# Performance work log

Hardware: AMD Instinct MI355X
Metric: run time of the kernel (lower is better)

The kernel has to match this reference:

```python
import jax, jax.numpy as jnp
from jax import lax
import numpy as np

H = W = 2048
C = 3
KSIZE = 2
SIGMA = 2.0
ITERATIONS = 2
RADII = (256.0, 768.0)
# with max_displacement=0 all circle centers coincide, so 'close to any circle'
# reduces to distance^2 < max(radius^2)
SRADII_MAX = max(r ** 2 for r in RADII)
SCLEAN_MAX = max(max(r - KSIZE, 0.0) ** 2 for r in RADII)


def _gaussian_blur(x, sigma):
    """skimage.filters.gaussian equivalent: separable gaussian, truncate=4.0,
    mode='nearest' (edge padding), channel_axis=-1 (no blur across channels)."""
    radius = int(4.0 * sigma + 0.5)
    t = np.arange(-radius, radius + 1, dtype=np.float32)
    k = np.exp(-0.5 * (t / sigma) ** 2)
    k = (k / k.sum()).astype(np.float32)
    for axis in (0, 1):
        pad = [(0, 0)] * x.ndim
        pad[axis] = (radius, radius)
        xp = jnp.pad(x, pad, mode='edge')
        n = x.shape[axis]
        acc = jnp.zeros_like(x)
        for j in range(k.shape[0]):
            acc = acc + k[j] * lax.slice_in_dim(xp, j, j + n, axis=axis)
        x = acc
    return x


def _glass_forward(img, offsets):
    r = KSIZE
    Hv = H - 2 * r + 1  # loop range(r, H-r+1) -> H-2r+1 rows
    Wv = W - 2 * r + 1
    HWtot = H * W
    # original quirk: cx = shape[0]//2 compared against column index w,
    # cy = shape[1]//2 against row index h; identical for a square image.
    cx = H // 2
    cy = W // 2
    ys = jnp.arange(r, H - r + 1)
    xs = jnp.arange(r, W - r + 1)
    HH, WW = jnp.meshgrid(ys, xs, indexing='ij')  # (Hv, Wv)
    d2 = (cx - WW) ** 2 + (cy - HH) ** 2
    swap_mask = (d2 >= SRADII_MAX).reshape(-1)  # swap only OUTSIDE all circles
    local = ((HH - r) * Wv + (WW - r)).reshape(-1)  # raster order within loop
    lin = (HH * W + WW).reshape(-1)

    # Every read in the original swap loop comes from array_orig (never
    # updated), so the final value of each pixel equals array_orig[source]
    # where source is determined by the LAST write targeting that pixel.
    # Each loop step emits two ordered writes:
    #   array[h, w]   = orig[h_, w_]   (order = 2*raster)
    #   array[h_, w_] = orig[h, w]    (order = 2*raster + 1)
    # We replay this exactly with a scatter-max over write order.
    writes = []
    for i in range(ITERATIONS):
        dh = offsets[i, :, :, 0]
        dw = offsets[i, :, :, 1]
        lin_ = ((HH + dh) * W + (WW + dw)).reshape(-1)
        base = i * 2 * Hv * Wv
        o1 = base + 2 * local
        o2 = o1 + 1
        writes.append((lin, lin_, o1))
        writes.append((lin_, lin, o2))

    win = jnp.full((HWtot,), -1, jnp.int32)
    for tgt, src_idx, order in writes:
        win = win.at[tgt].max(jnp.where(swap_mask, order, -1))
    src = jnp.full((HWtot,), -1, jnp.int32)
    for tgt, src_idx, order in writes:
        hit = swap_mask & (order == win[tgt])
        src = src.at[tgt].max(jnp.where(hit, src_idx, -1))

    orig_flat = img.reshape(HWtot, C)
    gathered = orig_flat[jnp.maximum(src, 0)]
    swapped = jnp.where((src >= 0)[:, None], gathered, orig_flat).reshape(H, W, C)

    blurred = jnp.clip(_gaussian_blur(swapped / 255.0, SIGMA), 0.0, 1.0) * 255.0

    # restore original pixels close to the shrunken (clean) circles
    clean = d2 < SCLEAN_MAX  # (Hv, Wv)
    clean_full = jnp.zeros((H, W), bool).at[r:H - r + 1, r:W - r + 1].set(clean)
    return jnp.where(clean_full[:, :, None], img, blurred)


def setup_inputs() -> dict:
    key = jax.random.key(0)
    k1, k2 = jax.random.split(key)
    img = jax.random.uniform(k1, (H, W, C), jnp.float32) * 255.0
    offsets = jax.random.randint(
        k2, (ITERATIONS, H - 2 * KSIZE + 1, W - 2 * KSIZE + 1, 2),
        -KSIZE, KSIZE, dtype=jnp.int32)
    return {"img": img, "offsets": offsets}


def reference(img, offsets):
    return _glass_forward(img, offsets)
```

## Files before the change

### kernel.cpp

```cpp
#include <hip/hip_runtime.h>
#include <hip/hip_fp16.h>

#define Hh 2048
#define Ww 2048
#define HW (2048 * 2048)
constexpr int REG = 2045;
constexpr int RBASE = 2 * 2045 * 2045;
constexpr int SWAP_D2 = 589824;
constexpr int CLEAN_D2 = 586756;

__device__ __constant__ float GK[17] = {
    6.691628e-05f, 4.363490e-04f, 2.215963e-03f, 8.764304e-03f,
    2.699596e-02f, 6.475994e-02f, 1.209875e-01f, 1.760358e-01f,
    1.9947466e-01f, 1.760358e-01f, 1.209875e-01f, 6.475994e-02f,
    2.699596e-02f, 8.764304e-03f, 2.215963e-03f, 4.363490e-04f,
    6.691628e-05f};

constexpr int TX = 32, TY = 8;
constexpr int HX = TX + 3, HY = TY + 3;

__global__ __launch_bounds__(256) void swap_gather(
    const float* __restrict__ img, const int* __restrict__ off,
    __half* __restrict__ A) {
  int x0 = blockIdx.x * TX, y0 = blockIdx.y * TY;
  int tx = threadIdx.x & 31, ty = threadIdx.x >> 5;
  int px = x0 + tx, py = y0 + ty;
  int plin = py * Ww + px;
  int src = plin;

  int mxx = max(abs(1024 - (x0 - 1)), abs(1024 - (x0 + TX + 1)));
  int mxy = max(abs(1024 - (y0 - 1)), abs(1024 - (y0 + TY + 1)));
  if (mxx * mxx + mxy * mxy >= SWAP_D2) {
    __shared__ int4 sh[HY * HX];
    for (int e = threadIdx.x; e < HY * HX; e += 256) {
      int ly = e / HX, lx = e - ly * HX;
      int qy = y0 - 1 + ly, qx = x0 - 1 + lx;
      int4 v = make_int4(100, 100, 100, 100);
      int dcx = 1024 - qx, dcy = 1024 - qy;
      if (qy >= 2 && qy <= 2046 && qx >= 2 && qx <= 2046 &&
          dcx * dcx + dcy * dcy >= SWAP_D2) {
        int base = ((qy - 2) * REG + (qx - 2)) * 2;
        const int2 a0 = *(const int2*)&off[base];
        const int2 a1 = *(const int2*)&off[RBASE + base];
        v = make_int4(a0.x, a0.y, a1.x, a1.y);
      }
      sh[e] = v;
    }
    __syncthreads();

    int best = -1;
    int base0 = 2 * ((py - 2) * REG + (px - 2)) + 1;
    {
      int dcx = 1024 - px, dcy = 1024 - py;
      if (px >= 2 && px <= 2046 && py >= 2 && py <= 2046 &&
          dcx * dcx + dcy * dcy >= SWAP_D2) {
        best = RBASE + base0 - 1;
        int4 v = sh[(ty + 1) * HX + (tx + 1)];
        src = plin + v.z * Ww + v.w;
      }
    }
#pragma unroll
    for (int dyi = 0; dyi < 4; ++dyi) {
      int ddy = 1 - dyi;
#pragma unroll
      for (int dxi = 0; dxi < 4; ++dxi) {
        int ddx = 1 - dxi;
        int4 v = sh[(ty + dyi) * HX + (tx + dxi)];
        int ordc = base0 - 2 * (ddy * REG + ddx);
        int qlin = plin - ddy * Ww - ddx;
        bool h0 = (v.x == ddy) & (v.y == ddx);
        bool h1 = (v.z == ddy) & (v.w == ddx);
        if (h0 & (ordc > best)) { best = ordc; src = qlin; }
        int ord1 = ordc + RBASE;
        if (h1 & (ord1 > best)) { best = ord1; src = qlin; }
      }
    }
  }

  float r = img[src * 3 + 0];
  float g = img[src * 3 + 1];
  float b = img[src * 3 + 2];
  A[plin] = __float2half(r);
  A[HW + plin] = __float2half(g);
  A[2 * HW + plin] = __float2half(b);
}

constexpr int YPT = 16;
__global__ void vblur(const __half* __restrict__ A, __half* __restrict__ B) {
  int x0 = (blockIdx.x * 256 + threadIdx.x) * 2;
  int y0 = blockIdx.y * YPT;
  const __half* Ap = A + (size_t)blockIdx.z * HW;
  __half* Bp = B + (size_t)blockIdx.z * HW;
  float2 acc[YPT];
#pragma unroll
  for (int k = 0; k < YPT; ++k) acc[k] = make_float2(0.f, 0.f);
#pragma unroll
  for (int j = 0; j < YPT + 16; ++j) {
    int ys = y0 - 8 + j;
    ys = ys < 0 ? 0 : (ys > Hh - 1 ? Hh - 1 : ys);
    __half2 h = *(const __half2*)&Ap[ys * Ww + x0];
    float2 v = __half22float2(h);
#pragma unroll
    for (int k = 0; k < YPT; ++k) {
      int t = j - k;
      if (t >= 0 && t <= 16) {
        acc[k].x += GK[t] * v.x;
        acc[k].y += GK[t] * v.y;
      }
    }
  }
#pragma unroll
  for (int k = 0; k < YPT; ++k) {
    *(__half2*)&Bp[(y0 + k) * Ww + x0] = __float22half2_rn(acc[k]);
  }
}

__global__ void hblur_compose(const __half* __restrict__ B,
                              const float* __restrict__ img,
                              float* __restrict__ out) {
  __shared__ float tile[256 + 16];
  int tid = threadIdx.x;
  int xs = blockIdx.x * 256;
  int y = blockIdx.y;
  int x = xs + tid;
  float br[3];
  for (int c = 0; c < 3; ++c) {
    const __half* Bp = B + (size_t)c * HW + (size_t)y * Ww;
    __syncthreads();
    int xg = xs - 8 + tid;
    xg = xg < 0 ? 0 : (xg > Ww - 1 ? Ww - 1 : xg);
    tile[tid] = __half2float(Bp[xg]);
    if (tid < 16) {
      int xg2 = xs - 8 + 256 + tid;
      xg2 = xg2 > Ww - 1 ? Ww - 1 : xg2;
      tile[256 + tid] = __half2float(Bp[xg2]);
    }
    __syncthreads();
    float s = 0.f;
#pragma unroll
    for (int j = 0; j < 17; ++j) s += GK[j] * tile[tid + j];
    br[c] = s;
  }
  int dx = 1024 - x, dy = 1024 - y;
  int d2 = dx * dx + dy * dy;
  bool clean = (x >= 2 && x <= 2046 && y >= 2 && y <= 2046 && d2 < CLEAN_D2);
  int p3 = (y * Ww + x) * 3;
  if (clean) {
    out[p3 + 0] = img[p3 + 0];
    out[p3 + 1] = img[p3 + 1];
    out[p3 + 2] = img[p3 + 2];
  } else {
#pragma unroll
    for (int c = 0; c < 3; ++c) {
      float v = br[c];
      v = v < 0.f ? 0.f : (v > 255.f ? 255.f : v);
      out[p3 + c] = v;
    }
  }
}

extern "C" void kernel_launch(void* const* d_in, const int* in_sizes, int n_in,
                              void* d_out, int out_size, void* d_ws,
                              size_t ws_size, hipStream_t stream) {
  const float* img = (const float*)d_in[0];
  const int* off = (const int*)d_in[1];
  float* out = (float*)d_out;

  __half* A = (__half*)d_ws;
  __half* Bp = A + (size_t)3 * HW;

  swap_gather<<<dim3(Ww / TX, Hh / TY), 256, 0, stream>>>(img, off, A);
  vblur<<<dim3(4, Hh / YPT, 3), 256, 0, stream>>>(A, Bp);
  hblur_compose<<<dim3(Ww / 256, Hh), 256, 0, stream>>>(Bp, img, out);
}
```

Baseline: 187.5 us.

## Pack swap offsets into bytes, order-based candidate scan, widen blur vectors

```diff
diff --git a/kernel.cpp b/kernel.cpp
--- a/kernel.cpp
+++ b/kernel.cpp
@@ -26,57 +26,67 @@
   int tx = threadIdx.x & 31, ty = threadIdx.x >> 5;
   int px = x0 + tx, py = y0 + ty;
   int plin = py * Ww + px;
-  int src = plin;
+  int srcoff = 0;
 
   int mxx = max(abs(1024 - (x0 - 1)), abs(1024 - (x0 + TX + 1)));
   int mxy = max(abs(1024 - (y0 - 1)), abs(1024 - (y0 + TY + 1)));
   if (mxx * mxx + mxy * mxy >= SWAP_D2) {
-    __shared__ int4 sh[HY * HX];
+    __shared__ unsigned sh[HY * HX];
     for (int e = threadIdx.x; e < HY * HX; e += 256) {
       int ly = e / HX, lx = e - ly * HX;
       int qy = y0 - 1 + ly, qx = x0 - 1 + lx;
-      int4 v = make_int4(100, 100, 100, 100);
+      unsigned v = 0xFFFFFFFFu;
       int dcx = 1024 - qx, dcy = 1024 - qy;
       if (qy >= 2 && qy <= 2046 && qx >= 2 && qx <= 2046 &&
           dcx * dcx + dcy * dcy >= SWAP_D2) {
         int base = ((qy - 2) * REG + (qx - 2)) * 2;
         const int2 a0 = *(const int2*)&off[base];
         const int2 a1 = *(const int2*)&off[RBASE + base];
-        v = make_int4(a0.x, a0.y, a1.x, a1.y);
+        v = (unsigned)(a0.y + 2) | ((unsigned)(a0.x + 2) << 8) |
+            ((unsigned)(a1.y + 2) << 16) | ((unsigned)(a1.x + 2) << 24);
       }
       sh[e] = v;
     }
     __syncthreads();
 
-    int best = -1;
-    int base0 = 2 * ((py - 2) * REG + (px - 2)) + 1;
+    unsigned w[4][4];
+#pragma unroll
+    for (int dyi = 0; dyi < 4; ++dyi)
+#pragma unroll
+      for (int dxi = 0; dxi < 4; ++dxi)
+        w[dyi][dxi] = sh[(ty + dyi) * HX + (tx + dxi)];
+
+#define CANDC(dyi, dxi) ((unsigned)((1 - (dxi)) + 2) | ((unsigned)((1 - (dyi)) + 2) << 8))
+#define OFFC(dyi, dxi) (-(1 - (dyi)) * Ww - (1 - (dxi)))
+#define CAND0(dyi, dxi) \
+  if ((w[dyi][dxi] & 0xFFFFu) == CANDC(dyi, dxi)) srcoff = OFFC(dyi, dxi);
+#define CAND1(dyi, dxi) \
+  if ((w[dyi][dxi] >> 16) == CANDC(dyi, dxi)) srcoff = OFFC(dyi, dxi);
+
+    CAND0(0, 0) CAND0(0, 1) CAND0(0, 2) CAND0(0, 3)
+    CAND0(1, 0) CAND0(1, 1) CAND0(1, 2) CAND0(1, 3)
+    CAND0(2, 0) CAND0(2, 1) CAND0(2, 2) CAND0(2, 3)
+    CAND0(3, 0) CAND0(3, 1) CAND0(3, 2) CAND0(3, 3)
+    CAND1(0, 0) CAND1(0, 1) CAND1(0, 2) CAND1(0, 3)
+    CAND1(1, 0)
     {
-      int dcx = 1024 - px, dcy = 1024 - py;
-      if (px >= 2 && px <= 2046 && py >= 2 && py <= 2046 &&
-          dcx * dcx + dcy * dcy >= SWAP_D2) {
-        best = RBASE + base0 - 1;
-        int4 v = sh[(ty + 1) * HX + (tx + 1)];
-        src = plin + v.z * Ww + v.w;
-      }
-    }
-#pragma unroll
-    for (int dyi = 0; dyi < 4; ++dyi) {
-      int ddy = 1 - dyi;
-#pragma unroll
-      for (int dxi = 0; dxi < 4; ++dxi) {
-        int ddx = 1 - dxi;
-        int4 v = sh[(ty + dyi) * HX + (tx + dxi)];
-        int ordc = base0 - 2 * (ddy * REG + ddx);
-        int qlin = plin - ddy * Ww - ddx;
-        bool h0 = (v.x == ddy) & (v.y == ddx);
-        bool h1 = (v.z == ddy) & (v.w == ddx);
-        if (h0 & (ordc > best)) { best = ordc; src = qlin; }
-        int ord1 = ordc + RBASE;
-        if (h1 & (ord1 > best)) { best = ord1; src = qlin; }
-      }
-    }
-  }
-
+      unsigned wc = w[1][1];
+      if ((wc >> 24) != 0xFFu) {
+        int dh1 = (int)((wc >> 24) & 0xFFu) - 2;
+        int dw1 = (int)((wc >> 16) & 0xFFu) - 2;
+        srcoff = dh1 * Ww + dw1;
+      }
+    }
+    CAND1(1, 1) CAND1(1, 2) CAND1(1, 3)
+    CAND1(2, 0) CAND1(2, 1) CAND1(2, 2) CAND1(2, 3)
+    CAND1(3, 0) CAND1(3, 1) CAND1(3, 2) CAND1(3, 3)
+#undef CANDC
+#undef OFFC
+#undef CAND0
+#undef CAND1
+  }
+
+  int src = plin + srcoff;
   float r = img[src * 3 + 0];
   float g = img[src * 3 + 1];
   float b = img[src * 3 + 2];
@@ -86,75 +96,114 @@
 }
 
 constexpr int YPT = 16;
-__global__ void vblur(const __half* __restrict__ A, __half* __restrict__ B) {
-  int x0 = (blockIdx.x * 256 + threadIdx.x) * 2;
-  int y0 = blockIdx.y * YPT;
-  const __half* Ap = A + (size_t)blockIdx.z * HW;
-  __half* Bp = B + (size_t)blockIdx.z * HW;
-  float2 acc[YPT];
-#pragma unroll
-  for (int k = 0; k < YPT; ++k) acc[k] = make_float2(0.f, 0.f);
+__global__ __launch_bounds__(256) void vblur(const __half* __restrict__ A,
+                                             __half* __restrict__ B) {
+  int b = blockIdx.x;
+  int xcd = b & 7, r = b >> 3;
+  int ystrip = (xcd << 4) | (r & 15);
+  int rem = r >> 4;
+  int xb = rem & 1, c = rem >> 1;
+  int x0 = (xb * 256 + threadIdx.x) * 4;
+  int y0 = ystrip * YPT;
+  const __half* Ap = A + (size_t)c * HW;
+  __half* Bp = B + (size_t)c * HW;
+
+  float acc[YPT][4];
+#pragma unroll
+  for (int k = 0; k < YPT; ++k)
+#pragma unroll
+    for (int q = 0; q < 4; ++q) acc[k][q] = 0.f;
+
 #pragma unroll
   for (int j = 0; j < YPT + 16; ++j) {
     int ys = y0 - 8 + j;
     ys = ys < 0 ? 0 : (ys > Hh - 1 ? Hh - 1 : ys);
-    __half2 h = *(const __half2*)&Ap[ys * Ww + x0];
-    float2 v = __half22float2(h);
+    uint2 raw = *(const uint2*)&Ap[(size_t)ys * Ww + x0];
+    __half2 h01 = *(__half2*)&raw.x;
+    __half2 h23 = *(__half2*)&raw.y;
+    float2 v01 = __half22float2(h01);
+    float2 v23 = __half22float2(h23);
 #pragma unroll
     for (int k = 0; k < YPT; ++k) {
       int t = j - k;
       if (t >= 0 && t <= 16) {
-        acc[k].x += GK[t] * v.x;
-        acc[k].y += GK[t] * v.y;
+        float gk = GK[t];
+        acc[k][0] += gk * v01.x;
+        acc[k][1] += gk * v01.y;
+        acc[k][2] += gk * v23.x;
+        acc[k][3] += gk * v23.y;
       }
     }
   }
 #pragma unroll
   for (int k = 0; k < YPT; ++k) {
-    *(__half2*)&Bp[(y0 + k) * Ww + x0] = __float22half2_rn(acc[k]);
-  }
-}
-
-__global__ void hblur_compose(const __half* __restrict__ B,
-                              const float* __restrict__ img,
-                              float* __restrict__ out) {
-  __shared__ float tile[256 + 16];
+    uint2 o;
+    __half2 h01 = __float22half2_rn(make_float2(acc[k][0], acc[k][1]));
+    __half2 h23 = __float22half2_rn(make_float2(acc[k][2], acc[k][3]));
+    o.x = *(unsigned*)&h01;
+    o.y = *(unsigned*)&h23;
+    *(uint2*)&Bp[(size_t)(y0 + k) * Ww + x0] = o;
+  }
+}
+
+__global__ __launch_bounds__(256) void hblur_compose(
+    const __half* __restrict__ B, const float* __restrict__ img,
+    float* __restrict__ out) {
+  __shared__ float tile[528 + 1];
   int tid = threadIdx.x;
-  int xs = blockIdx.x * 256;
+  int xs = blockIdx.x * 512;
   int y = blockIdx.y;
-  int x = xs + tid;
-  float br[3];
+  float br[3][2];
+
   for (int c = 0; c < 3; ++c) {
     const __half* Bp = B + (size_t)c * HW + (size_t)y * Ww;
     __syncthreads();
-    int xg = xs - 8 + tid;
-    xg = xg < 0 ? 0 : (xg > Ww - 1 ? Ww - 1 : xg);
-    tile[tid] = __half2float(Bp[xg]);
-    if (tid < 16) {
-      int xg2 = xs - 8 + 256 + tid;
-      xg2 = xg2 > Ww - 1 ? Ww - 1 : xg2;
-      tile[256 + tid] = __half2float(Bp[xg2]);
+    for (int e = tid; e < 264; e += 256) {
+      int xg = xs - 8 + 2 * e;
+      float2 v;
+      if (xg >= 0 && xg + 1 <= Ww - 1) {
+        __half2 h = *(const __half2*)&Bp[xg];
+        v = __half22float2(h);
+      } else {
+        int xlo = xg < 0 ? 0 : (xg > Ww - 1 ? Ww - 1 : xg);
+        int xhi = xg + 1 < 0 ? 0 : (xg + 1 > Ww - 1 ? Ww - 1 : xg + 1);
+        v = make_float2(__half2float(Bp[xlo]), __half2float(Bp[xhi]));
+      }
+      *(float2*)&tile[2 * e] = v;
     }
     __syncthreads();
-    float s = 0.f;
-#pragma unroll
-    for (int j = 0; j < 17; ++j) s += GK[j] * tile[tid + j];
-    br[c] = s;
-  }
-  int dx = 1024 - x, dy = 1024 - y;
-  int d2 = dx * dx + dy * dy;
-  bool clean = (x >= 2 && x <= 2046 && y >= 2 && y <= 2046 && d2 < CLEAN_D2);
-  int p3 = (y * Ww + x) * 3;
-  if (clean) {
-    out[p3 + 0] = img[p3 + 0];
-    out[p3 + 1] = img[p3 + 1];
-    out[p3 + 2] = img[p3 + 2];
-  } else {
-#pragma unroll
-    for (int c = 0; c < 3; ++c) {
-      float v = br[c];
-      v = v < 0.f ? 0.f : (v > 255.f ? 255.f : v);
-      out[p3 + c] = v;
+    float f[19];
+#pragma unroll
+    for (int j = 0; j < 19; ++j) f[j] = tile[2 * tid + j];
+    float s0 = 0.f, s1 = 0.f;
+#pragma unroll
+    for (int j = 0; j < 17; ++j) {
+      s0 += GK[j] * f[j];
+      s1 += GK[j] * f[j + 1];
+    }
+    br[c][0] = s0;
+    br[c][1] = s1;
+  }
+
+  int x = xs + 2 * tid;
+#pragma unroll
+  for (int u = 0; u < 2; ++u) {
+    int xu = x + u;
+    int dx = 1024 - xu, dy = 1024 - y;
+    bool clean = (xu >= 2 && xu <= 2046 && y >= 2 && y <= 2046 &&
+                  dx * dx + dy * dy < CLEAN_D2);
+    int p3 = (y * Ww + xu) * 3;
+    if (clean) {
+      out[p3 + 0] = img[p3 + 0];
+      out[p3 + 1] = img[p3 + 1];
+      out[p3 + 2] = img[p3 + 2];
+    } else {
+#pragma unroll
+      for (int c = 0; c < 3; ++c) {
+        float v = br[c][u];
+        v = v < 0.f ? 0.f : (v > 255.f ? 255.f : v);
+        out[p3 + c] = v;
+      }
     }
   }
 }
@@ -170,6 +219,6 @@
   __half* Bp = A + (size_t)3 * HW;
 
   swap_gather<<<dim3(Ww / TX, Hh / TY), 256, 0, stream>>>(img, off, A);
-  vblur<<<dim3(4, Hh / YPT, 3), 256, 0, stream>>>(A, Bp);
-  hblur_compose<<<dim3(Ww / 256, Hh), 256, 0, stream>>>(Bp, img, out);
-}
+  vblur<<<768, 256, 0, stream>>>(A, Bp);
+  hblur_compose<<<dim3(Ww / 512, Hh), 256, 0, stream>>>(Bp, img, out);
+}
```

Result: faster. 179.5 us (-4.3%).

## Fuse vertical and horizontal blur into one tiled kernel and vectorize swap gather

Applied to the files above, without the earlier changes.

```diff
diff --git a/kernel.cpp b/kernel.cpp
--- a/kernel.cpp
+++ b/kernel.cpp
@@ -16,145 +16,207 @@
     2.699596e-02f, 8.764304e-03f, 2.215963e-03f, 4.363490e-04f,
     6.691628e-05f};
 
-constexpr int TX = 32, TY = 8;
+struct F3 { float x, y, z; };
+
+constexpr int TX = 64, TY = 16;
 constexpr int HX = TX + 3, HY = TY + 3;
 
 __global__ __launch_bounds__(256) void swap_gather(
     const float* __restrict__ img, const int* __restrict__ off,
     __half* __restrict__ A) {
   int x0 = blockIdx.x * TX, y0 = blockIdx.y * TY;
-  int tx = threadIdx.x & 31, ty = threadIdx.x >> 5;
-  int px = x0 + tx, py = y0 + ty;
+  int tx4 = (threadIdx.x & 15) * 4, ty = threadIdx.x >> 4;
+  int px = x0 + tx4, py = y0 + ty;
   int plin = py * Ww + px;
-  int src = plin;
 
   int mxx = max(abs(1024 - (x0 - 1)), abs(1024 - (x0 + TX + 1)));
   int mxy = max(abs(1024 - (y0 - 1)), abs(1024 - (y0 + TY + 1)));
-  if (mxx * mxx + mxy * mxy >= SWAP_D2) {
-    __shared__ int4 sh[HY * HX];
-    for (int e = threadIdx.x; e < HY * HX; e += 256) {
-      int ly = e / HX, lx = e - ly * HX;
-      int qy = y0 - 1 + ly, qx = x0 - 1 + lx;
-      int4 v = make_int4(100, 100, 100, 100);
-      int dcx = 1024 - qx, dcy = 1024 - qy;
-      if (qy >= 2 && qy <= 2046 && qx >= 2 && qx <= 2046 &&
-          dcx * dcx + dcy * dcy >= SWAP_D2) {
-        int base = ((qy - 2) * REG + (qx - 2)) * 2;
-        const int2 a0 = *(const int2*)&off[base];
-        const int2 a1 = *(const int2*)&off[RBASE + base];
-        v = make_int4(a0.x, a0.y, a1.x, a1.y);
+  if (mxx * mxx + mxy * mxy < SWAP_D2) {
+    const float4 c0 = *(const float4*)(img + (size_t)plin * 3);
+    const float4 c1 = *(const float4*)(img + (size_t)plin * 3 + 4);
+    const float4 c2 = *(const float4*)(img + (size_t)plin * 3 + 8);
+    float v[12] = {c0.x, c0.y, c0.z, c0.w, c1.x, c1.y, c1.z, c1.w,
+                   c2.x, c2.y, c2.z, c2.w};
+#pragma unroll
+    for (int c = 0; c < 3; ++c) {
+      __half2 h01 = __float22half2_rn(make_float2(v[c], v[3 + c]));
+      __half2 h23 = __float22half2_rn(make_float2(v[6 + c], v[9 + c]));
+      uint2 o = make_uint2(*(unsigned*)&h01, *(unsigned*)&h23);
+      *(uint2*)&A[(size_t)c * HW + plin] = o;
+    }
+    return;
+  }
+
+  __shared__ unsigned sh[HY * HX];
+  for (int e = threadIdx.x; e < HY * HX; e += 256) {
+    int ly = e / HX, lx = e - ly * HX;
+    int qy = y0 - 1 + ly, qx = x0 - 1 + lx;
+    unsigned v = 0xFFFFFFFFu;
+    int dcx = 1024 - qx, dcy = 1024 - qy;
+    if (qy >= 2 && qy <= 2046 && qx >= 2 && qx <= 2046 &&
+        dcx * dcx + dcy * dcy >= SWAP_D2) {
+      int base = ((qy - 2) * REG + (qx - 2)) * 2;
+      const int2 a0 = *(const int2*)&off[base];
+      const int2 a1 = *(const int2*)&off[RBASE + base];
+      v = (unsigned)(a0.y + 2) | ((unsigned)(a0.x + 2) << 8) |
+          ((unsigned)(a1.y + 2) << 16) | ((unsigned)(a1.x + 2) << 24);
+    }
+    sh[e] = v;
+  }
+  __syncthreads();
+
+  unsigned w[4][7];
+#pragma unroll
+  for (int dyi = 0; dyi < 4; ++dyi)
+#pragma unroll
+    for (int c = 0; c < 7; ++c) w[dyi][c] = sh[(ty + dyi) * HX + tx4 + c];
+
+  int so[4] = {0, 0, 0, 0};
+
+#define CANDC(dyi, dxi) \
+  ((unsigned)((1 - (dxi)) + 2) | ((unsigned)((1 - (dyi)) + 2) << 8))
+#define OFFC(dyi, dxi) (-(1 - (dyi)) * Ww - (1 - (dxi)))
+#define C0(j, dyi, dxi) \
+  if ((w[dyi][(j) + (dxi)] & 0xFFFFu) == CANDC(dyi, dxi)) so[j] = OFFC(dyi, dxi);
+#define C1(j, dyi, dxi) \
+  if ((w[dyi][(j) + (dxi)] >> 16) == CANDC(dyi, dxi)) so[j] = OFFC(dyi, dxi);
+#define PXSEQ(j)                                                        \
+  C0(j, 0, 0) C0(j, 0, 1) C0(j, 0, 2) C0(j, 0, 3)                       \
+  C0(j, 1, 0) C0(j, 1, 1) C0(j, 1, 2) C0(j, 1, 3)                       \
+  C0(j, 2, 0) C0(j, 2, 1) C0(j, 2, 2) C0(j, 2, 3)                       \
+  C0(j, 3, 0) C0(j, 3, 1) C0(j, 3, 2) C0(j, 3, 3)                       \
+  C1(j, 0, 0) C1(j, 0, 1) C1(j, 0, 2) C1(j, 0, 3)                       \
+  C1(j, 1, 0)                                                           \
+  { unsigned wc = w[1][(j) + 1];                                        \
+    if ((wc >> 24) != 0xFFu) {                                          \
+      int dh1 = (int)((wc >> 24) & 0xFFu) - 2;                          \
+      int dw1 = (int)((wc >> 16) & 0xFFu) - 2;                          \
+      so[j] = dh1 * Ww + dw1; } }                                       \
+  C1(j, 1, 1) C1(j, 1, 2) C1(j, 1, 3)                                   \
+  C1(j, 2, 0) C1(j, 2, 1) C1(j, 2, 2) C1(j, 2, 3)                       \
+  C1(j, 3, 0) C1(j, 3, 1) C1(j, 3, 2) C1(j, 3, 3)
+
+  PXSEQ(0) PXSEQ(1) PXSEQ(2) PXSEQ(3)
+#undef CANDC
+#undef OFFC
+#undef C0
+#undef C1
+#undef PXSEQ
+
+  F3 g[4];
+#pragma unroll
+  for (int j = 0; j < 4; ++j)
+    g[j] = *(const F3*)(img + (size_t)(plin + j + so[j]) * 3);
+  {
+    __half2 h01 = __float22half2_rn(make_float2(g[0].x, g[1].x));
+    __half2 h23 = __float22half2_rn(make_float2(g[2].x, g[3].x));
+    *(uint2*)&A[plin] = make_uint2(*(unsigned*)&h01, *(unsigned*)&h23);
+  }
+  {
+    __half2 h01 = __float22half2_rn(make_float2(g[0].y, g[1].y));
+    __half2 h23 = __float22half2_rn(make_float2(g[2].y, g[3].y));
+    *(uint2*)&A[HW + plin] = make_uint2(*(unsigned*)&h01, *(unsigned*)&h23);
+  }
+  {
+    __half2 h01 = __float22half2_rn(make_float2(g[0].z, g[1].z));
+    __half2 h23 = __float22half2_rn(make_float2(g[2].z, g[3].z));
+    *(uint2*)&A[2 * HW + plin] = make_uint2(*(unsigned*)&h01, *(unsigned*)&h23);
+  }
+}
+
+constexpr int BTX = 112, BTY = 32;
+constexpr int SROWS = BTY + 16;
+constexpr int SCOLU = 64;
+constexpr int MSTR = 130;
+
+__global__ __launch_bounds__(256) void blur_compose(
+    const __half* __restrict__ A, const float* __restrict__ img,
+    float* __restrict__ out) {
+  __shared__ unsigned sIn[SROWS * SCOLU];
+  __shared__ float sMid[BTY * MSTR];
+  int x0 = blockIdx.x * BTX;
+  int y0 = blockIdx.y * BTY;
+  int tid = threadIdx.x;
+  int cu = tid & 63, rg = tid >> 6;
+  int rr = tid >> 3, cg = tid & 7;
+
+  for (int c = 0; c < 3; ++c) {
+    const __half* Ap = A + (size_t)c * HW;
+    __syncthreads();
+#pragma unroll
+    for (int k = 0; k < 12; ++k) {
+      int e = tid + k * 256;
+      int row = e >> 6, u = e & 63;
+      int gy = y0 - 8 + row;
+      gy = gy < 0 ? 0 : (gy > Hh - 1 ? Hh - 1 : gy);
+      int gx = x0 - 8 + 2 * u;
+      unsigned v;
+      if (gx >= 0 && gx + 1 <= Ww - 1) {
+        v = *(const unsigned*)&Ap[(size_t)gy * Ww + gx];
+      } else {
+        int xlo = gx < 0 ? 0 : (gx > Ww - 1 ? Ww - 1 : gx);
+        int xg1 = gx + 1;
+        int xhi = xg1 < 0 ? 0 : (xg1 > Ww - 1 ? Ww - 1 : xg1);
+        __half2 h;
+        h.x = Ap[(size_t)gy * Ww + xlo];
+        h.y = Ap[(size_t)gy * Ww + xhi];
+        v = *(unsigned*)&h;
       }
-      sh[e] = v;
+      sIn[e] = v;
     }
     __syncthreads();
-
-    int best = -1;
-    int base0 = 2 * ((py - 2) * REG + (px - 2)) + 1;
-    {
-      int dcx = 1024 - px, dcy = 1024 - py;
-      if (px >= 2 && px <= 2046 && py >= 2 && py <= 2046 &&
-          dcx * dcx + dcy * dcy >= SWAP_D2) {
-        best = RBASE + base0 - 1;
-        int4 v = sh[(ty + 1) * HX + (tx + 1)];
-        src = plin + v.z * Ww + v.w;
+    float acc[8][2];
+#pragma unroll
+    for (int r = 0; r < 8; ++r) acc[r][0] = acc[r][1] = 0.f;
+#pragma unroll
+    for (int j = 0; j < 24; ++j) {
+      unsigned raw = sIn[(rg * 8 + j) * SCOLU + cu];
+      float2 v = __half22float2(*(__half2*)&raw);
+#pragma unroll
+      for (int r = 0; r < 8; ++r) {
+        int t = j - r;
+        if (t >= 0 && t <= 16) {
+          acc[r][0] += GK[t] * v.x;
+          acc[r][1] += GK[t] * v.y;
+        }
       }
     }
 #pragma unroll
-    for (int dyi = 0; dyi < 4; ++dyi) {
-      int ddy = 1 - dyi;
-#pragma unroll
-      for (int dxi = 0; dxi < 4; ++dxi) {
-        int ddx = 1 - dxi;
-        int4 v = sh[(ty + dyi) * HX + (tx + dxi)];
-        int ordc = base0 - 2 * (ddy * REG + ddx);
-        int qlin = plin - ddy * Ww - ddx;
-        bool h0 = (v.x == ddy) & (v.y == ddx);
-        bool h1 = (v.z == ddy) & (v.w == ddx);
-        if (h0 & (ordc > best)) { best = ordc; src = qlin; }
-        int ord1 = ordc + RBASE;
-        if (h1 & (ord1 > best)) { best = ord1; src = qlin; }
+    for (int r = 0; r < 8; ++r) {
+      *(float2*)&sMid[(rg * 8 + r) * MSTR + 2 * cu] =
+          make_float2(acc[r][0], acc[r][1]);
+    }
+    __syncthreads();
+    int y = y0 + rr;
+    const float* srow = &sMid[rr * MSTR + cg * 14];
+    float f[30];
+#pragma unroll
+    for (int j = 0; j < 15; ++j) {
+      float2 v = *(const float2*)&srow[2 * j];
+      f[2 * j] = v.x;
+      f[2 * j + 1] = v.y;
+    }
+    int dyc = 1024 - y;
+    bool yok = (y >= 2 && y <= 2046);
+#pragma unroll
+    for (int k = 0; k < 14; ++k) {
+      int x = x0 + cg * 14 + k;
+      if (x < Ww) {
+        float s = 0.f;
+#pragma unroll
+        for (int j = 0; j < 17; ++j) s += GK[j] * f[k + j];
+        int dxc = 1024 - x;
+        bool clean =
+            yok && x >= 2 && x <= 2046 && dxc * dxc + dyc * dyc < CLEAN_D2;
+        int p3 = (y * Ww + x) * 3 + c;
+        float vout;
+        if (clean) {
+          vout = img[p3];
+        } else {
+          vout = s < 0.f ? 0.f : (s > 255.f ? 255.f : s);
+        }
+        out[p3] = vout;
       }
-    }
-  }
-
-  float r = img[src * 3 + 0];
-  float g = img[src * 3 + 1];
-  float b = img[src * 3 + 2];
-  A[plin] = __float2half(r);
-  A[HW + plin] = __float2half(g);
-  A[2 * HW + plin] = __float2half(b);
-}
-
-constexpr int YPT = 16;
-__global__ void vblur(const __half* __restrict__ A, __half* __restrict__ B) {
-  int x0 = (blockIdx.x * 256 + threadIdx.x) * 2;
-  int y0 = blockIdx.y * YPT;
-  const __half* Ap = A + (size_t)blockIdx.z * HW;
-  __half* Bp = B + (size_t)blockIdx.z * HW;
-  float2 acc[YPT];
-#pragma unroll
-  for (int k = 0; k < YPT; ++k) acc[k] = make_float2(0.f, 0.f);
-#pragma unroll
-  for (int j = 0; j < YPT + 16; ++j) {
-    int ys = y0 - 8 + j;
-    ys = ys < 0 ? 0 : (ys > Hh - 1 ? Hh - 1 : ys);
-    __half2 h = *(const __half2*)&Ap[ys * Ww + x0];
-    float2 v = __half22float2(h);
-#pragma unroll
-    for (int k = 0; k < YPT; ++k) {
-      int t = j - k;
-      if (t >= 0 && t <= 16) {
-        acc[k].x += GK[t] * v.x;
-        acc[k].y += GK[t] * v.y;
-      }
-    }
-  }
-#pragma unroll
-  for (int k = 0; k < YPT; ++k) {
-    *(__half2*)&Bp[(y0 + k) * Ww + x0] = __float22half2_rn(acc[k]);
-  }
-}
-
-__global__ void hblur_compose(const __half* __restrict__ B,
-                              const float* __restrict__ img,
-                              float* __restrict__ out) {
-  __shared__ float tile[256 + 16];
-  int tid = threadIdx.x;
-  int xs = blockIdx.x * 256;
-  int y = blockIdx.y;
-  int x = xs + tid;
-  float br[3];
-  for (int c = 0; c < 3; ++c) {
-    const __half* Bp = B + (size_t)c * HW + (size_t)y * Ww;
-    __syncthreads();
-    int xg = xs - 8 + tid;
-    xg = xg < 0 ? 0 : (xg > Ww - 1 ? Ww - 1 : xg);
-    tile[tid] = __half2float(Bp[xg]);
-    if (tid < 16) {
-      int xg2 = xs - 8 + 256 + tid;
-      xg2 = xg2 > Ww - 1 ? Ww - 1 : xg2;
-      tile[256 + tid] = __half2float(Bp[xg2]);
-    }
-    __syncthreads();
-    float s = 0.f;
-#pragma unroll
-    for (int j = 0; j < 17; ++j) s += GK[j] * tile[tid + j];
-    br[c] = s;
-  }
-  int dx = 1024 - x, dy = 1024 - y;
-  int d2 = dx * dx + dy * dy;
-  bool clean = (x >= 2 && x <= 2046 && y >= 2 && y <= 2046 && d2 < CLEAN_D2);
-  int p3 = (y * Ww + x) * 3;
-  if (clean) {
-    out[p3 + 0] = img[p3 + 0];
-    out[p3 + 1] = img[p3 + 1];
-    out[p3 + 2] = img[p3 + 2];
-  } else {
-#pragma unroll
-    for (int c = 0; c < 3; ++c) {
-      float v = br[c];
-      v = v < 0.f ? 0.f : (v > 255.f ? 255.f : v);
-      out[p3 + c] = v;
     }
   }
 }
@@ -167,9 +229,8 @@
   float* out = (float*)d_out;
 
   __half* A = (__half*)d_ws;
-  __half* Bp = A + (size_t)3 * HW;
 
   swap_gather<<<dim3(Ww / TX, Hh / TY), 256, 0, stream>>>(img, off, A);
-  vblur<<<dim3(4, Hh / YPT, 3), 256, 0, stream>>>(A, Bp);
-  hblur_compose<<<dim3(Ww / 256, Hh), 256, 0, stream>>>(Bp, img, out);
+  blur_compose<<<dim3((Ww + BTX - 1) / BTX, Hh / BTY), 256, 0, stream>>>(
+      A, img, out);
 }
```

Result: slower. 337.5 us (+80.0%).
